# Optimization experiments

Hardware: AMD Instinct MI355X
Metric: run time of the kernel (lower is better)

Reference implementation:

```python
import jax, jax.numpy as jnp
import numpy as np

SR = 16000
NYQ = SR / 2.0
N_FFT = 400
HOP = 160
WIN = 400
OUT_CHANNELS = 64
OUTPUT_SIZE = 64
MIN_LOW_HZ = 50.0
MIN_BAND_HZ = 50.0
FRAME_LENGTH = 400
EPS_LN = 1e-5


def _to_mel(hz):
    return 2595.0 * np.log10(1.0 + hz / 700.0)


def _to_hz(mel):
    return 700.0 * (10.0 ** (mel / 2595.0) - 1.0)


def setup_inputs() -> dict:
    key = jax.random.key(0)
    k1, = jax.random.split(key, 1)
    waveforms = jax.random.normal(k1, (1024, 1, 16000), dtype=jnp.float32)
    # mel-spaced init, exactly as in __init__ (freq_init='mel', range_constraint=False)
    low_hz = 30.0
    high_hz = NYQ - (MIN_LOW_HZ + MIN_BAND_HZ)
    mel = np.linspace(_to_mel(low_hz), _to_mel(high_hz), OUT_CHANNELS + 1)
    hz = _to_hz(mel)
    low_hz_ = jnp.asarray(hz[:-1], dtype=jnp.float32).reshape(-1, 1)
    band_hz_ = jnp.asarray(np.diff(hz), dtype=jnp.float32).reshape(-1, 1)
    ln_weight = jnp.ones((OUT_CHANNELS, 1), dtype=jnp.float32)
    ln_bias = jnp.zeros((OUT_CHANNELS, 1), dtype=jnp.float32)
    return {
        "waveforms": waveforms,
        "low_hz_": low_hz_,
        "band_hz_": band_hz_,
        "ln_weight": ln_weight,
        "ln_bias": ln_bias,
    }


def _hann_periodic(n):
    # torch.hann_window default: periodic=True
    k = jnp.arange(n, dtype=jnp.float32)
    return 0.5 - 0.5 * jnp.cos(2.0 * jnp.pi * k / n)


def _stft_mag(x):
    pad = N_FFT // 2
    xp = jnp.pad(x, ((0, 0), (pad, pad)), mode="reflect")
    n_frames = 1 + (xp.shape[1] - N_FFT) // HOP
    idx = jnp.arange(n_frames)[:, None] * HOP + jnp.arange(N_FFT)[None, :]
    frames = xp[:, idx] * _hann_periodic(WIN)  # [B, F_t, n_fft]
    spec = jnp.fft.rfft(frames, axis=-1)       # [B, F_t, n_fft//2+1]
    return jnp.abs(spec).transpose(0, 2, 1)    # [B, n_fft//2+1, F_t]


def _get_filters(low_hz_, band_hz_):
    # vectorized over all channels (original loops per channel)
    low = MIN_LOW_HZ + jnp.abs(low_hz_)                                   # [C,1]
    high = jnp.clip(low + MIN_BAND_HZ + jnp.abs(band_hz_), MIN_LOW_HZ, NYQ)
    freq = jnp.linspace(0.0, NYQ, N_FFT // 2 + 1, dtype=jnp.float32)      # [F]
    mask = (freq >= low) & (freq <= high)                                 # [C,F]
    center = (low + high) / 2.0
    bw = high - low
    resp = 1.0 - jnp.abs(freq - center) / (bw / 2.0)                      # triangular
    return jnp.where(mask, resp, 0.0)                                     # [C,F]


def _gln(x, weight, bias):
    # GlobalLayerNorm over dims (1,2) of [B,C,T]
    mean = jnp.mean(x, axis=(1, 2), keepdims=True)
    var = jnp.mean((x - mean) ** 2, axis=(1, 2), keepdims=True)
    return weight * (x - mean) / jnp.sqrt(var + EPS_LN) + bias


def _interp_linear(x, out_size):
    # torch F.interpolate(mode='linear', align_corners=False) along last dim
    t_in = x.shape[-1]
    scale = t_in / out_size
    pos = (jnp.arange(out_size, dtype=jnp.float32) + 0.5) * scale - 0.5
    pos = jnp.clip(pos, 0.0, t_in - 1)
    i0 = jnp.floor(pos).astype(jnp.int32)
    i1 = jnp.minimum(i0 + 1, t_in - 1)
    w = (pos - i0.astype(jnp.float32))
    return x[..., i0] * (1.0 - w) + x[..., i1] * w


def reference(waveforms, low_hz_, band_hz_, ln_weight, ln_bias):
    B = waveforms.shape[0]
    target_length = HOP * (OUTPUT_SIZE - 1) + FRAME_LENGTH  # 10480
    cur = waveforms.shape[-1]
    x = waveforms[:, 0, :]
    if target_length > cur:  # static shape decision
        x = jnp.pad(x, ((0, 0), (0, target_length - cur)))
    mag_spec = _stft_mag(x)                       # [B, 201, F_t]
    filters = _get_filters(low_hz_, band_hz_)     # [C, 201]
    filtered = jnp.einsum("cf,bft->bct", filters, mag_spec)  # [B, C, F_t]
    filtered = _gln(filtered, ln_weight, ln_bias)
    energy = filtered ** 2
    log_energy = jnp.log10(energy + 1e-6)         # [B, C, F_t]
    if log_energy.shape[-1] != OUTPUT_SIZE:
        log_energy = _interp_linear(log_energy, OUTPUT_SIZE)  # [B, C, 64]
    log_energy = log_energy[:, None, :, :].transpose(0, 1, 3, 2)  # [B,1,64,C]
    return (log_energy, filters)
```

## Files before the change

### kernel.cpp

```cpp
#include <hip/hip_runtime.h>
#include <math.h>

#define BLOCK 512
#define JMAX 13

typedef __attribute__((ext_vector_type(8))) short short8;
typedef __attribute__((ext_vector_type(16))) float f32x16;
typedef __attribute__((ext_vector_type(4))) unsigned uint4v;

__device__ inline unsigned short f2bf(float x) {
    unsigned u = __float_as_uint(x);
    unsigned r = u + 0x7fffu + ((u >> 16) & 1u);
    return (unsigned short)(r >> 16);
}

__global__ void fse_filters(const float* __restrict__ low_hz_,
                            const float* __restrict__ band_hz_,
                            float* __restrict__ out)
{
    int idx = blockIdx.x * 256 + threadIdx.x;
    if (idx >= 64 * 201) return;
    int c = idx / 201;
    int k = idx - c * 201;
    float lo = 50.0f + fabsf(low_hz_[c]);
    float hi = lo + 50.0f + fabsf(band_hz_[c]);
    hi = fminf(fmaxf(hi, 50.0f), 8000.0f);
    float ctr = 0.5f * (lo + hi);
    float hbw = 0.5f * (hi - lo);
    float fq = 40.0f * (float)k;
    float resp = 1.0f - fabsf(fq - ctr) / hbw;
    out[idx] = (fq >= lo && fq <= hi) ? resp : 0.0f;
}

__global__ void fse_setup_B(unsigned short* __restrict__ bt)
{
    int idx = blockIdx.x * 256 + threadIdx.x;
    if (idx >= 372736) return;
    int e   = idx & 7;
    int t   = idx >> 3;
    int row = t % 448;
    int q   = t / 448;
    int p   = q & 3;
    int pl  = (q >> 2) & 1;
    int kc  = q >> 3;
    int n   = kc * 32 + p * 8 + e;
    float v = 0.0f;
    if (n < 400) {
        int bin = -1, isim = 0;
        if (row <= 200) bin = row;
        else if (row >= 224 && row <= 424) { bin = row - 224; isim = 1; }
        if (bin >= 0) {
            int a = (bin * n) % 400;
            float th = 6.283185307179586f * ((float)a / 400.0f);
            float sn, cs;
            sincosf(th, &sn, &cs);
            float wn = 0.5f - 0.5f * cosf(6.283185307179586f * ((float)n / 400.0f));
            v = isim ? (-wn * sn) : (wn * cs);
        }
    }
    unsigned short h = f2bf(v);
    float hf = __uint_as_float((unsigned)h << 16);
    unsigned short l = f2bf(v - hf);
    bt[idx] = pl ? l : h;
}

__global__ __launch_bounds__(512, 2)
void fse_main_mfma(const float* __restrict__ wav,
                   const float* __restrict__ low_hz_,
                   const float* __restrict__ band_hz_,
                   const float* __restrict__ ln_w,
                   const float* __restrict__ ln_b,
                   const unsigned short* __restrict__ Bt,
                   float* __restrict__ out)
{
    __shared__ __align__(16) char smem[114688];
    float* mags = (float*)smem;
    float* fbuf = (float*)(smem + 84032);

    __shared__ float fctr[64], finv[64];
    __shared__ int   fks[64], fke[64];
    __shared__ float red[8];
    __shared__ float stats[2];

    const int b    = blockIdx.x;
    const int tid  = threadIdx.x;
    const int w    = tid >> 6;
    const int lane = tid & 63;
    const float* __restrict__ x = wav + b * 16000;

    if (tid < 64) {
        float lo = 50.0f + fabsf(low_hz_[tid]);
        float hi = lo + 50.0f + fabsf(band_hz_[tid]);
        hi = fminf(fmaxf(hi, 50.0f), 8000.0f);
        float ctr = 0.5f * (lo + hi);
        float hbw = 0.5f * (hi - lo);
        int ks = (int)ceilf(lo * 0.025f);
        if (ks < 0) ks = 0;
        while (40.0f * (float)ks < lo) ++ks;
        while (ks > 0 && 40.0f * (float)(ks - 1) >= lo) --ks;
        int ke = (int)floorf(hi * 0.025f);
        if (ke > 200) ke = 200;
        while (40.0f * (float)ke > hi) --ke;
        while (ke < 200 && 40.0f * (float)(ke + 1) <= hi) ++ke;
        fctr[tid] = ctr;
        finv[tid] = (hbw > 0.0f) ? (1.0f / hbw) : 0.0f;
        fks[tid]  = ks;
        fke[tid]  = ke;
    }

    const int mt   = w >> 1;
    const int half = w & 1;
    const int jrow = lane & 31;
    const int g    = lane >> 5;
    const int arow = mt * 32 + jrow;
    const int te   = (arow <= 100) ? arow : 50;

    const uint4* __restrict__ btg = (const uint4*)Bt;

    {
        uint4 rr[7];
        #pragma unroll
        for (int i = 0; i < 7; ++i) rr[i] = btg[i * 512 + tid];
        uint4* dst = (uint4*)smem;
        #pragma unroll
        for (int i = 0; i < 7; ++i) dst[i * 512 + tid] = rr[i];
    }
    __syncthreads();

    f32x16 acc[7];
    #pragma unroll
    for (int n = 0; n < 7; ++n) {
        #pragma unroll
        for (int e = 0; e < 16; ++e) acc[n][e] = 0.0f;
    }

    int curoff = 0;
    for (int kc = 0; kc < 13; ++kc) {
        uint4 rr[7];
        const bool pre = (kc < 12);
        if (pre) {
            const uint4* src = btg + (kc + 1) * 3584;
            #pragma unroll
            for (int i = 0; i < 7; ++i) rr[i] = src[i * 512 + tid];
        }
        const unsigned short* bs = (const unsigned short*)(smem + curoff);

        #pragma unroll
        for (int s = 0; s < 2; ++s) {
            float v8[8];
            int i0 = 160 * te - 200 + kc * 32 + s * 16 + g * 8;
            if (i0 >= 0 && i0 <= 15992) {
                float4 a0 = *(const float4*)(x + i0);
                float4 a1 = *(const float4*)(x + i0 + 4);
                v8[0] = a0.x; v8[1] = a0.y; v8[2] = a0.z; v8[3] = a0.w;
                v8[4] = a1.x; v8[5] = a1.y; v8[6] = a1.z; v8[7] = a1.w;
            } else {
                #pragma unroll
                for (int e = 0; e < 8; ++e) {
                    int p = i0 + e;
                    p = (p < 0) ? -p : p;
                    p = (p > 15999) ? (31998 - p) : p;
                    v8[e] = x[p];
                }
            }
            uint4v ah, al;
            #pragma unroll
            for (int qq = 0; qq < 4; ++qq) {
                unsigned short h0 = f2bf(v8[2*qq]),   h1 = f2bf(v8[2*qq+1]);
                float hf0 = __uint_as_float((unsigned)h0 << 16);
                float hf1 = __uint_as_float((unsigned)h1 << 16);
                unsigned short l0 = f2bf(v8[2*qq] - hf0), l1 = f2bf(v8[2*qq+1] - hf1);
                ah[qq] = (unsigned)h0 | ((unsigned)h1 << 16);
                al[qq] = (unsigned)l0 | ((unsigned)l1 << 16);
            }
            short8 Ah = __builtin_bit_cast(short8, ah);
            short8 Al = __builtin_bit_cast(short8, al);

            const int pb = (s * 2 + g) * 448;
            #pragma unroll
            for (int n = 0; n < 7; ++n) {
                const int ro = (half * 7 + n) * 32 + jrow;
                short8 Bh = *(const short8*)(bs + (pb + ro) * 8);
                short8 Bl = *(const short8*)(bs + (1792 * 8) + (pb + ro) * 8);
                acc[n] = __builtin_amdgcn_mfma_f32_32x32x16_bf16(Ah, Bh, acc[n], 0, 0, 0);
                acc[n] = __builtin_amdgcn_mfma_f32_32x32x16_bf16(Ah, Bl, acc[n], 0, 0, 0);
                acc[n] = __builtin_amdgcn_mfma_f32_32x32x16_bf16(Al, Bh, acc[n], 0, 0, 0);
            }
        }

        if (pre) {
            uint4* dst = (uint4*)(smem + (curoff ^ 57344));
            #pragma unroll
            for (int i = 0; i < 7; ++i) dst[i * 512 + tid] = rr[i];
        }
        __syncthreads();
        curoff ^= 57344;
    }

    if (half == 0) {
        #pragma unroll
        for (int n = 0; n < 7; ++n) {
            int k = n * 32 + jrow;
            if (k <= 200) {
                #pragma unroll
                for (int r = 0; r < 16; ++r) {
                    int t = mt * 32 + (r & 3) + 8 * (r >> 2) + 4 * g;
                    if (t <= 100) mags[t * 208 + k] = acc[n][r];
                }
            }
        }
    }
    __syncthreads();
    if (half == 1) {
        #pragma unroll
        for (int n = 0; n < 7; ++n) {
            int k = n * 32 + jrow;
            if (k <= 200) {
                #pragma unroll
                for (int r = 0; r < 16; ++r) {
                    int t = mt * 32 + (r & 3) + 8 * (r >> 2) + 4 * g;
                    if (t <= 100) {
                        float re = mags[t * 208 + k];
                        float im = acc[n][r];
                        mags[t * 208 + k] = sqrtf(re * re + im * im);
                    }
                }
            }
        }
    }
    __syncthreads();

    const float cctr = fctr[lane];
    const float cinv = finv[lane];
    const int   cks  = fks[lane];
    const int   cke  = fke[lane];
    for (int j = 0; j < JMAX; ++j) {
        int t = w + 8 * j;
        if (t > 100) break;
        float a2 = 0.0f;
        for (int k = cks; k <= cke; ++k) {
            float resp = 1.0f - fabsf(40.0f * (float)k - cctr) * cinv;
            a2 = fmaf(resp, mags[t * 208 + k], a2);
        }
        fbuf[lane * 101 + t] = a2;
    }
    __syncthreads();

    float s = 0.0f;
    for (int i = tid; i < 6464; i += BLOCK) s += fbuf[i];
    #pragma unroll
    for (int off = 32; off > 0; off >>= 1) s += __shfl_down(s, off, 64);
    if (lane == 0) red[w] = s;
    __syncthreads();
    if (tid == 0) {
        float tsum = 0.0f;
        for (int i = 0; i < 8; ++i) tsum += red[i];
        stats[0] = tsum * (1.0f / 6464.0f);
    }
    __syncthreads();
    const float mu = stats[0];
    float v = 0.0f;
    for (int i = tid; i < 6464; i += BLOCK) { float d = fbuf[i] - mu; v = fmaf(d, d, v); }
    #pragma unroll
    for (int off = 32; off > 0; off >>= 1) v += __shfl_down(v, off, 64);
    if (lane == 0) red[w] = v;
    __syncthreads();
    if (tid == 0) {
        float tsum = 0.0f;
        for (int i = 0; i < 8; ++i) tsum += red[i];
        stats[1] = tsum * (1.0f / 6464.0f);
    }
    __syncthreads();
    const float var  = stats[1];
    const float isig = 1.0f / sqrtf(var + 1e-5f);

    for (int idx = tid; idx < 4096; idx += BLOCK) {
        const int to = idx >> 6;
        const int c  = idx & 63;
        float pos = ((float)to + 0.5f) * 1.578125f - 0.5f;
        pos = fminf(fmaxf(pos, 0.0f), 100.0f);
        int i0 = (int)floorf(pos);
        int i1 = i0 + 1; if (i1 > 100) i1 = 100;
        float fr = pos - (float)i0;
        float wc = ln_w[c], bc = ln_b[c];
        float x0 = fbuf[c * 101 + i0];
        float x1 = fbuf[c * 101 + i1];
        float y0 = fmaf(wc, (x0 - mu) * isig, bc);
        float y1 = fmaf(wc, (x1 - mu) * isig, bc);
        float l0 = log10f(fmaf(y0, y0, 1e-6f));
        float l1 = log10f(fmaf(y1, y1, 1e-6f));
        out[b * 4096 + idx] = l0 * (1.0f - fr) + l1 * fr;
    }
}

__global__ __launch_bounds__(512, 2)
void fse_main_valu(const float* __restrict__ wav,
                   const float* __restrict__ low_hz_,
                   const float* __restrict__ band_hz_,
                   const float* __restrict__ ln_w,
                   const float* __restrict__ ln_b,
                   float* __restrict__ out)
{
    __shared__ float  xp[16400];
    __shared__ float2 Xs[8][204];
    __shared__ float  mags[8][204];
    __shared__ float  fbuf[64 * 101];
    __shared__ float  fctr[64], finv[64];
    __shared__ int    fks[64], fke[64];
    __shared__ float  red[8];
    __shared__ float  stats[2];

    const int b    = blockIdx.x;
    const int tid  = threadIdx.x;
    const int w    = tid >> 6;
    const int lane = tid & 63;
    const float* __restrict__ x = wav + b * 16000;

    for (int i = tid; i < 16400; i += BLOCK) {
        int p = i - 200;
        p = (p < 0) ? -p : p;
        p = (p > 15999) ? (31998 - p) : p;
        xp[i] = x[p];
    }
    if (tid < 64) {
        float lo = 50.0f + fabsf(low_hz_[tid]);
        float hi = lo + 50.0f + fabsf(band_hz_[tid]);
        hi = fminf(fmaxf(hi, 50.0f), 8000.0f);
        float ctr = 0.5f * (lo + hi);
        float hbw = 0.5f * (hi - lo);
        int ks = (int)ceilf(lo * 0.025f);
        if (ks < 0) ks = 0;
        while (40.0f * (float)ks < lo) ++ks;
        while (ks > 0 && 40.0f * (float)(ks - 1) >= lo) --ks;
        int ke = (int)floorf(hi * 0.025f);
        if (ke > 200) ke = 200;
        while (40.0f * (float)ke > hi) --ke;
        while (ke < 200 && 40.0f * (float)(ke + 1) <= hi) ++ke;
        fctr[tid] = ctr;
        finv[tid] = (hbw > 0.0f) ? (1.0f / hbw) : 0.0f;
        fks[tid]  = ks;
        fke[tid]  = ke;
    }
    __syncthreads();

    const float cctr = fctr[lane];
    const float cinv = finv[lane];
    const int   cks  = fks[lane];
    const int   cke  = fke[lane];

    float reX[4][JMAX], imX[4][JMAX];
    const float2* __restrict__ xp2 = (const float2*)xp;
    float c0[4], s0[4], c1[4], s1[4], cd[4], sd[4];
    #pragma unroll
    for (int m = 0; m < 4; ++m) {
        const int k = m * 64 + lane;
        const float th = -0.015707963267948966f * (float)k;
        sincosf(th, &s1[m], &c1[m]);
        sincosf(th + th, &sd[m], &cd[m]);
        c0[m] = 1.0f; s0[m] = 0.0f;
        #pragma unroll
        for (int j = 0; j < JMAX; ++j) { reX[m][j] = 0.0f; imX[m][j] = 0.0f; }
    }
    const int o12 = (w < 5) ? 640 * 12 : 0;
    int ib = 80 * w;
    #pragma unroll 2
    for (int h = 0; h < 200; ++h) {
        #pragma unroll
        for (int j = 0; j < JMAX; ++j) {
            const int off = (j == 12) ? o12 : 640 * j;
            float2 f = xp2[ib + off];
            #pragma unroll
            for (int m = 0; m < 4; ++m) {
                reX[m][j] = fmaf(f.x, c0[m], reX[m][j]);
                imX[m][j] = fmaf(f.x, s0[m], imX[m][j]);
                reX[m][j] = fmaf(f.y, c1[m], reX[m][j]);
                imX[m][j] = fmaf(f.y, s1[m], imX[m][j]);
            }
        }
        #pragma unroll
        for (int m = 0; m < 4; ++m) {
            float nc0 = fmaf(c0[m], cd[m], -(s0[m] * sd[m]));
            float ns0 = fmaf(s0[m], cd[m],  (c0[m] * sd[m]));
            float nc1 = fmaf(c1[m], cd[m], -(s1[m] * sd[m]));
            float ns1 = fmaf(s1[m], cd[m],  (c1[m] * sd[m]));
            c0[m] = nc0; s0[m] = ns0; c1[m] = nc1; s1[m] = ns1;
        }
        ++ib;
    }

    float2* __restrict__ myX   = &Xs[w][0];
    float*  __restrict__ mymag = &mags[w][0];
    for (int j = 0; j < JMAX; ++j) {
        const int t = w + 8 * j;
        if (t > 100) break;
        #pragma unroll
        for (int m = 0; m < 4; ++m) {
            const int k = m * 64 + lane;
            if (k < 202) myX[k] = make_float2(reX[m][j], imX[m][j]);
        }
        asm volatile("s_waitcnt lgkmcnt(0)" ::: "memory");
        #pragma unroll
        for (int m = 0; m < 4; ++m) {
            const int k = m * 64 + lane;
            if (k <= 200) {
                float2 xm = (k == 0) ? myX[1] : myX[k - 1];
                float imm = (k == 0) ? -xm.y : xm.y;
                float2 xq = myX[k + 1];
                float rw = 0.5f * reX[m][j] - 0.25f * (xm.x + xq.x);
                float iw = 0.5f * imX[m][j] - 0.25f * (imm  + xq.y);
                mymag[k] = sqrtf(rw * rw + iw * iw);
            }
        }
        asm volatile("s_waitcnt lgkmcnt(0)" ::: "memory");
        float acc = 0.0f;
        for (int k = cks; k <= cke; ++k) {
            float resp = 1.0f - fabsf(40.0f * (float)k - cctr) * cinv;
            acc = fmaf(resp, mymag[k], acc);
        }
        fbuf[lane * 101 + t] = acc;
    }
    __syncthreads();

    float s = 0.0f;
    for (int i = tid; i < 6464; i += BLOCK) s += fbuf[i];
    #pragma unroll
    for (int off = 32; off > 0; off >>= 1) s += __shfl_down(s, off, 64);
    if (lane == 0) red[w] = s;
    __syncthreads();
    if (tid == 0) {
        float tsum = 0.0f;
        for (int i = 0; i < 8; ++i) tsum += red[i];
        stats[0] = tsum * (1.0f / 6464.0f);
    }
    __syncthreads();
    const float mu = stats[0];
    float v = 0.0f;
    for (int i = tid; i < 6464; i += BLOCK) { float d = fbuf[i] - mu; v = fmaf(d, d, v); }
    #pragma unroll
    for (int off = 32; off > 0; off >>= 1) v += __shfl_down(v, off, 64);
    if (lane == 0) red[w] = v;
    __syncthreads();
    if (tid == 0) {
        float tsum = 0.0f;
        for (int i = 0; i < 8; ++i) tsum += red[i];
        stats[1] = tsum * (1.0f / 6464.0f);
    }
    __syncthreads();
    const float var  = stats[1];
    const float isig = 1.0f / sqrtf(var + 1e-5f);

    for (int idx = tid; idx < 4096; idx += BLOCK) {
        const int to = idx >> 6;
        const int c  = idx & 63;
        float pos = ((float)to + 0.5f) * 1.578125f - 0.5f;
        pos = fminf(fmaxf(pos, 0.0f), 100.0f);
        int i0 = (int)floorf(pos);
        int i1 = i0 + 1; if (i1 > 100) i1 = 100;
        float fr = pos - (float)i0;
        float wc = ln_w[c], bc = ln_b[c];
        float x0 = fbuf[c * 101 + i0];
        float x1 = fbuf[c * 101 + i1];
        float y0 = fmaf(wc, (x0 - mu) * isig, bc);
        float y1 = fmaf(wc, (x1 - mu) * isig, bc);
        float l0 = log10f(fmaf(y0, y0, 1e-6f));
        float l1 = log10f(fmaf(y1, y1, 1e-6f));
        out[b * 4096 + idx] = l0 * (1.0f - fr) + l1 * fr;
    }
}

extern "C" void kernel_launch(void* const* d_in, const int* in_sizes, int n_in,
                              void* d_out, int out_size, void* d_ws, size_t ws_size,
                              hipStream_t stream)
{
    const float* wav = (const float*)d_in[0];
    const float* lo  = (const float*)d_in[1];
    const float* bd  = (const float*)d_in[2];
    const float* lw  = (const float*)d_in[3];
    const float* lb  = (const float*)d_in[4];
    float* out = (float*)d_out;

    fse_filters<<<(64 * 201 + 255) / 256, 256, 0, stream>>>(lo, bd, out + 1024 * 4096);

    const size_t BNEED = (size_t)372736 * sizeof(unsigned short);
    if (ws_size >= BNEED) {
        unsigned short* Bts = (unsigned short*)d_ws;
        fse_setup_B<<<(372736 + 255) / 256, 256, 0, stream>>>(Bts);
        fse_main_mfma<<<1024, BLOCK, 0, stream>>>(wav, lo, bd, lw, lb, Bts, out);
    } else {
        fse_main_valu<<<1024, BLOCK, 0, stream>>>(wav, lo, bd, lw, lb, out);
    }
}
```

Measured before the change: 246.5 us.

## Prefetch waveform tiles, pad mags stride, re-map filterbank, fuse LN stats

Global loads of the next waveform A-tile are issued one k-chunk ahead, next to the B-tile prefetch, so their latency overlaps the current MFMA work. The mags row stride changes from 208 to 209 to reduce LDS bank conflicts. The filterbank reduction is remapped so each lane handles time frames while a wave loops over channels. The layer-norm mean and variance are computed in one pass using sum and sum of squares. The single-pass variance is less numerically stable, and the extra prefetch registers add pressure under launch_bounds(512,2).

```diff
diff --git a/kernel.cpp b/kernel.cpp
--- a/kernel.cpp
+++ b/kernel.cpp
@@ -2,7 +2,7 @@
 #include <math.h>
 
 #define BLOCK 512
-#define JMAX 13
+#define MSTR 209
 
 typedef __attribute__((ext_vector_type(8))) short short8;
 typedef __attribute__((ext_vector_type(16))) float f32x16;
@@ -12,6 +12,44 @@
     unsigned u = __float_as_uint(x);
     unsigned r = u + 0x7fffu + ((u >> 16) & 1u);
     return (unsigned short)(r >> 16);
+}
+
+__device__ inline void splitA(const float* v, short8& Ah, short8& Al) {
+    uint4v ah, al;
+    #pragma unroll
+    for (int q = 0; q < 4; ++q) {
+        unsigned short h0 = f2bf(v[2*q]),   h1 = f2bf(v[2*q+1]);
+        float hf0 = __uint_as_float((unsigned)h0 << 16);
+        float hf1 = __uint_as_float((unsigned)h1 << 16);
+        unsigned short l0 = f2bf(v[2*q] - hf0), l1 = f2bf(v[2*q+1] - hf1);
+        ah[q] = (unsigned)h0 | ((unsigned)h1 << 16);
+        al[q] = (unsigned)l0 | ((unsigned)l1 << 16);
+    }
+    Ah = __builtin_bit_cast(short8, ah);
+    Al = __builtin_bit_cast(short8, al);
+}
+
+__device__ inline void loadA(const float* __restrict__ x, int te, int kc, int g,
+                             float* d0, float* d1) {
+    #pragma unroll
+    for (int s = 0; s < 2; ++s) {
+        float* d = s ? d1 : d0;
+        int i0 = 160 * te - 200 + kc * 32 + s * 16 + g * 8;
+        if (i0 >= 0 && i0 <= 15992) {
+            float4 a0 = *(const float4*)(x + i0);
+            float4 a1 = *(const float4*)(x + i0 + 4);
+            d[0] = a0.x; d[1] = a0.y; d[2] = a0.z; d[3] = a0.w;
+            d[4] = a1.x; d[5] = a1.y; d[6] = a1.z; d[7] = a1.w;
+        } else {
+            #pragma unroll
+            for (int e = 0; e < 8; ++e) {
+                int p = i0 + e;
+                p = (p < 0) ? -p : p;
+                p = (p > 15999) ? (31998 - p) : p;
+                d[e] = x[p];
+            }
+        }
+    }
 }
 
 __global__ void fse_filters(const float* __restrict__ low_hz_,
@@ -75,11 +113,11 @@
 {
     __shared__ __align__(16) char smem[114688];
     float* mags = (float*)smem;
-    float* fbuf = (float*)(smem + 84032);
+    float* fbuf = (float*)(smem + 84544);
 
     __shared__ float fctr[64], finv[64];
     __shared__ int   fks[64], fke[64];
-    __shared__ float red[8];
+    __shared__ float red[16];
     __shared__ float stats[2];
 
     const int b    = blockIdx.x;
@@ -117,6 +155,8 @@
 
     const uint4* __restrict__ btg = (const uint4*)Bt;
 
+    float ac[2][8], an[2][8];
+    loadA(x, te, 0, g, ac[0], ac[1]);
     {
         uint4 rr[7];
         #pragma unroll
@@ -136,55 +176,31 @@
 
     int curoff = 0;
     for (int kc = 0; kc < 13; ++kc) {
+        const bool pre = (kc < 12);
         uint4 rr[7];
-        const bool pre = (kc < 12);
         if (pre) {
             const uint4* src = btg + (kc + 1) * 3584;
             #pragma unroll
             for (int i = 0; i < 7; ++i) rr[i] = src[i * 512 + tid];
-        }
+            loadA(x, te, kc + 1, g, an[0], an[1]);
+        }
+
+        short8 Ah[2], Al[2];
+        splitA(ac[0], Ah[0], Al[0]);
+        splitA(ac[1], Ah[1], Al[1]);
+
         const unsigned short* bs = (const unsigned short*)(smem + curoff);
-
         #pragma unroll
         for (int s = 0; s < 2; ++s) {
-            float v8[8];
-            int i0 = 160 * te - 200 + kc * 32 + s * 16 + g * 8;
-            if (i0 >= 0 && i0 <= 15992) {
-                float4 a0 = *(const float4*)(x + i0);
-                float4 a1 = *(const float4*)(x + i0 + 4);
-                v8[0] = a0.x; v8[1] = a0.y; v8[2] = a0.z; v8[3] = a0.w;
-                v8[4] = a1.x; v8[5] = a1.y; v8[6] = a1.z; v8[7] = a1.w;
-            } else {
-                #pragma unroll
-                for (int e = 0; e < 8; ++e) {
-                    int p = i0 + e;
-                    p = (p < 0) ? -p : p;
-                    p = (p > 15999) ? (31998 - p) : p;
-                    v8[e] = x[p];
-                }
-            }
-            uint4v ah, al;
-            #pragma unroll
-            for (int qq = 0; qq < 4; ++qq) {
-                unsigned short h0 = f2bf(v8[2*qq]),   h1 = f2bf(v8[2*qq+1]);
-                float hf0 = __uint_as_float((unsigned)h0 << 16);
-                float hf1 = __uint_as_float((unsigned)h1 << 16);
-                unsigned short l0 = f2bf(v8[2*qq] - hf0), l1 = f2bf(v8[2*qq+1] - hf1);
-                ah[qq] = (unsigned)h0 | ((unsigned)h1 << 16);
-                al[qq] = (unsigned)l0 | ((unsigned)l1 << 16);
-            }
-            short8 Ah = __builtin_bit_cast(short8, ah);
-            short8 Al = __builtin_bit_cast(short8, al);
-
             const int pb = (s * 2 + g) * 448;
             #pragma unroll
             for (int n = 0; n < 7; ++n) {
                 const int ro = (half * 7 + n) * 32 + jrow;
                 short8 Bh = *(const short8*)(bs + (pb + ro) * 8);
-                short8 Bl = *(const short8*)(bs + (1792 * 8) + (pb + ro) * 8);
-                acc[n] = __builtin_amdgcn_mfma_f32_32x32x16_bf16(Ah, Bh, acc[n], 0, 0, 0);
-                acc[n] = __builtin_amdgcn_mfma_f32_32x32x16_bf16(Ah, Bl, acc[n], 0, 0, 0);
-                acc[n] = __builtin_amdgcn_mfma_f32_32x32x16_bf16(Al, Bh, acc[n], 0, 0, 0);
+                short8 Bl = *(const short8*)(bs + 14336 + (pb + ro) * 8);
+                acc[n] = __builtin_amdgcn_mfma_f32_32x32x16_bf16(Ah[s], Bh, acc[n], 0, 0, 0);
+                acc[n] = __builtin_amdgcn_mfma_f32_32x32x16_bf16(Ah[s], Bl, acc[n], 0, 0, 0);
+                acc[n] = __builtin_amdgcn_mfma_f32_32x32x16_bf16(Al[s], Bh, acc[n], 0, 0, 0);
             }
         }
 
@@ -194,6 +210,10 @@
             for (int i = 0; i < 7; ++i) dst[i * 512 + tid] = rr[i];
         }
         __syncthreads();
+        if (pre) {
+            #pragma unroll
+            for (int i = 0; i < 8; ++i) { ac[0][i] = an[0][i]; ac[1][i] = an[1][i]; }
+        }
         curoff ^= 57344;
     }
 
@@ -205,7 +225,7 @@
                 #pragma unroll
                 for (int r = 0; r < 16; ++r) {
                     int t = mt * 32 + (r & 3) + 8 * (r >> 2) + 4 * g;
-                    if (t <= 100) mags[t * 208 + k] = acc[n][r];
+                    if (t <= 100) mags[t * MSTR + k] = acc[n][r];
                 }
             }
         }
@@ -220,9 +240,9 @@
                 for (int r = 0; r < 16; ++r) {
                     int t = mt * 32 + (r & 3) + 8 * (r >> 2) + 4 * g;
                     if (t <= 100) {
-                        float re = mags[t * 208 + k];
+                        float re = mags[t * MSTR + k];
                         float im = acc[n][r];
-                        mags[t * 208 + k] = sqrtf(re * re + im * im);
+                        mags[t * MSTR + k] = sqrtf(re * re + im * im);
                     }
                 }
             }
@@ -230,49 +250,51 @@
     }
     __syncthreads();
 
-    const float cctr = fctr[lane];
-    const float cinv = finv[lane];
-    const int   cks  = fks[lane];
-    const int   cke  = fke[lane];
-    for (int j = 0; j < JMAX; ++j) {
-        int t = w + 8 * j;
-        if (t > 100) break;
-        float a2 = 0.0f;
-        for (int k = cks; k <= cke; ++k) {
-            float resp = 1.0f - fabsf(40.0f * (float)k - cctr) * cinv;
-            a2 = fmaf(resp, mags[t * 208 + k], a2);
-        }
-        fbuf[lane * 101 + t] = a2;
-    }
-    __syncthreads();
-
-    float s = 0.0f;
-    for (int i = tid; i < 6464; i += BLOCK) s += fbuf[i];
-    #pragma unroll
-    for (int off = 32; off > 0; off >>= 1) s += __shfl_down(s, off, 64);
-    if (lane == 0) red[w] = s;
+    {
+        const int t0 = lane;
+        const int t1v = 64 + lane;
+        const int t1 = (t1v <= 100) ? t1v : 100;
+        #pragma unroll
+        for (int i = 0; i < 8; ++i) {
+            const int c = w * 8 + i;
+            const float ctr = fctr[c];
+            const float inv = finv[c];
+            const int ks = fks[c], ke = fke[c];
+            float a0 = 0.0f, a1 = 0.0f;
+            for (int k = ks; k <= ke; ++k) {
+                float resp = 1.0f - fabsf(40.0f * (float)k - ctr) * inv;
+                a0 = fmaf(resp, mags[t0 * MSTR + k], a0);
+                a1 = fmaf(resp, mags[t1 * MSTR + k], a1);
+            }
+            fbuf[c * 101 + t0] = a0;
+            if (t1v <= 100) fbuf[c * 101 + t1v] = a1;
+        }
+    }
+    __syncthreads();
+
+    float s = 0.0f, ss = 0.0f;
+    for (int i = tid; i < 6464; i += BLOCK) {
+        float vv = fbuf[i];
+        s += vv;
+        ss = fmaf(vv, vv, ss);
+    }
+    #pragma unroll
+    for (int off = 32; off > 0; off >>= 1) {
+        s  += __shfl_down(s,  off, 64);
+        ss += __shfl_down(ss, off, 64);
+    }
+    if (lane == 0) { red[w] = s; red[8 + w] = ss; }
     __syncthreads();
     if (tid == 0) {
-        float tsum = 0.0f;
-        for (int i = 0; i < 8; ++i) tsum += red[i];
-        stats[0] = tsum * (1.0f / 6464.0f);
-    }
-    __syncthreads();
-    const float mu = stats[0];
-    float v = 0.0f;
-    for (int i = tid; i < 6464; i += BLOCK) { float d = fbuf[i] - mu; v = fmaf(d, d, v); }
-    #pragma unroll
-    for (int off = 32; off > 0; off >>= 1) v += __shfl_down(v, off, 64);
-    if (lane == 0) red[w] = v;
-    __syncthreads();
-    if (tid == 0) {
-        float tsum = 0.0f;
-        for (int i = 0; i < 8; ++i) tsum += red[i];
-        stats[1] = tsum * (1.0f / 6464.0f);
-    }
-    __syncthreads();
-    const float var  = stats[1];
-    const float isig = 1.0f / sqrtf(var + 1e-5f);
+        float ts = 0.0f, tss = 0.0f;
+        for (int i = 0; i < 8; ++i) { ts += red[i]; tss += red[8 + i]; }
+        float mu = ts * (1.0f / 6464.0f);
+        stats[0] = mu;
+        stats[1] = tss * (1.0f / 6464.0f) - mu * mu;
+    }
+    __syncthreads();
+    const float mu   = stats[0];
+    const float isig = 1.0f / sqrtf(stats[1] + 1e-5f);
 
     for (int idx = tid; idx < 4096; idx += BLOCK) {
         const int to = idx >> 6;
@@ -348,7 +370,7 @@
     const int   cks  = fks[lane];
     const int   cke  = fke[lane];
 
-    float reX[4][JMAX], imX[4][JMAX];
+    float reX[4][13], imX[4][13];
     const float2* __restrict__ xp2 = (const float2*)xp;
     float c0[4], s0[4], c1[4], s1[4], cd[4], sd[4];
     #pragma unroll
@@ -359,14 +381,14 @@
         sincosf(th + th, &sd[m], &cd[m]);
         c0[m] = 1.0f; s0[m] = 0.0f;
         #pragma unroll
-        for (int j = 0; j < JMAX; ++j) { reX[m][j] = 0.0f; imX[m][j] = 0.0f; }
+        for (int j = 0; j < 13; ++j) { reX[m][j] = 0.0f; imX[m][j] = 0.0f; }
     }
     const int o12 = (w < 5) ? 640 * 12 : 0;
     int ib = 80 * w;
     #pragma unroll 2
     for (int h = 0; h < 200; ++h) {
         #pragma unroll
-        for (int j = 0; j < JMAX; ++j) {
+        for (int j = 0; j < 13; ++j) {
             const int off = (j == 12) ? o12 : 640 * j;
             float2 f = xp2[ib + off];
             #pragma unroll
@@ -390,7 +412,7 @@
 
     float2* __restrict__ myX   = &Xs[w][0];
     float*  __restrict__ mymag = &mags[w][0];
-    for (int j = 0; j < JMAX; ++j) {
+    for (int j = 0; j < 13; ++j) {
         const int t = w + 8 * j;
         if (t > 100) break;
         #pragma unroll
```

New measurement: 352.5 us. +43.0%, slower.
